# Kernel optimization log

Measured on AMD Instinct MI355X. Metric: run time of the kernel, lower is better.

Reference implementation:

```python
import jax, jax.numpy as jnp
import numpy as np

EPS = 1e-5
SCALE = 0.25
H = 16  # num_heads

def _bn(x, gamma, beta):
    # training-mode BatchNorm1d over (batch, length) per channel; x: [M, C, N]
    mean = jnp.mean(x, axis=(0, 2), keepdims=True)
    var = jnp.var(x, axis=(0, 2), keepdims=True)
    return gamma[None, :, None] * (x - mean) * jax.lax.rsqrt(var + EPS) + beta[None, :, None]

def _spike(x, vth):
    # fresh MyNode within one forward: mem = 0/tau + x, spike if >= vth
    return (x >= vth).astype(x.dtype)

def setup_inputs() -> dict:
    key = jax.random.key(0)
    ks = jax.random.split(key, 8)
    T, B, C, N = 4, 1, 256, 1024
    x = jax.random.normal(ks[0], (T, B, C, N), dtype=jnp.float32)
    y = jax.random.normal(ks[1], (T, B, C, N), dtype=jnp.float32)
    def w(k):
        return jax.random.normal(k, (C, C), dtype=jnp.float32) * (1.0 / np.sqrt(C))
    return {
        "x": x, "y": y,
        "Wq": w(ks[2]), "gq": jnp.ones((C,), jnp.float32), "bq": jnp.zeros((C,), jnp.float32),
        "Wk": w(ks[3]), "gk": jnp.ones((C,), jnp.float32), "bk": jnp.zeros((C,), jnp.float32),
        "Wv": w(ks[4]), "gv": jnp.ones((C,), jnp.float32), "bv": jnp.zeros((C,), jnp.float32),
        "Wp": w(ks[5]), "gp": jnp.ones((C,), jnp.float32), "bp": jnp.zeros((C,), jnp.float32),
    }

def reference(x, y, Wq, gq, bq, Wk, gk, bk, Wv, gv, bv, Wp, gp, bp):
    T, B, C, N = x.shape
    D = C // H
    xf = x.reshape(T * B, C, N)
    yf = y.reshape(T * B, C, N)

    def branch(inp, W, g, b, vth):
        h = jnp.einsum('oc,mcn->mon', W, inp)      # conv1x1
        h = _bn(h, g, b)
        s = _spike(h, vth)                          # LIF spike (fresh state)
        # [T,B,C,N] -> split channels into heads -> [T,B,H,N,D]
        return s.reshape(T, B, H, D, N).transpose(0, 1, 2, 4, 3)

    q = branch(xf, Wq, gq, bq, 1.0)
    k = branch(yf, Wk, gk, bk, 1.0)
    v = branch(yf, Wv, gv, bv, 1.0)

    attn = jnp.einsum('tbhnd,tbhmd->tbhnm', q, k)   # [T,B,H,N,N]
    out = jnp.einsum('tbhnm,tbhmd->tbhnd', attn, v) * SCALE

    # [T,B,H,N,D] -> [T,B,C,N]
    out = out.transpose(0, 1, 2, 4, 3).reshape(T, B, C, N)
    out = _spike(out.reshape(T * B, C, N), 0.5)      # attn_lif, v_threshold=0.5
    out = jnp.einsum('oc,mcn->mon', Wp, out)         # proj conv1x1
    out = _spike(_bn(out, gp, bp), 1.0)              # proj_bn + proj_lif
    return out.reshape(T, B, C, N)
```

## Files before the change

### kernel.cpp

```cpp
#include <hip/hip_runtime.h>
#include <cstdint>
#include <cstddef>
#include <cmath>

static constexpr int C = 256;
static constexpr int N = 1024;
static constexpr int M = 4;
static constexpr size_t PLANE = (size_t)M * C * N;

typedef unsigned short u16;
typedef u16      u16x8 __attribute__((ext_vector_type(8)));
typedef u16      u16x4 __attribute__((ext_vector_type(4)));
typedef _Float16 f16x8 __attribute__((ext_vector_type(8)));
typedef float    f32x4 __attribute__((ext_vector_type(4)));

static constexpr int FSTR = 40;
static constexpr size_t LVX = (size_t)8 * 1024 * 256;
static constexpr size_t LVW = (size_t)4 * 256 * 256;


__device__ __forceinline__ void split3(float v, u16 &h0, u16 &h1, u16 &h2)
{
    union { _Float16 f; u16 u; } cv;
    float a0 = (fabsf(v) >= 6.103515625e-05f) ? v : 0.0f;
    cv.f = (_Float16)a0;                 h0 = cv.u;
    float f0 = (float)cv.f;
    float r1 = v - f0;
    cv.f = (_Float16)(r1 * 4096.0f);     h1 = cv.u;
    float f1 = (float)cv.f * 2.44140625e-4f;
    float r2 = r1 - f1;
    cv.f = (_Float16)(r2 * 16777216.0f); h2 = cv.u;
}

__global__ __launch_bounds__(256) void split_pre(
    const float* __restrict__ x, const float* __restrict__ y,
    const float* __restrict__ Wq, const float* __restrict__ Wk,
    const float* __restrict__ Wv, const float* __restrict__ Wp,
    u16* __restrict__ xyT, u16* __restrict__ wsp)
{
    const int z = blockIdx.z, tid = threadIdx.x;
    if (z < 8){
        const float* __restrict__ src = (z < 4) ? (x + (size_t)z * C * N)
                                                : (y + (size_t)(z - 4) * C * N);
        const int n0 = blockIdx.x * 64, c0 = blockIdx.y * 64;
        __shared__ float Ls[64][65];
        const int cr = tid >> 2, q = tid & 3;
        #pragma unroll
        for (int j = 0; j < 4; ++j){
            float4 vv = *(const float4*)(src + (size_t)(c0 + cr) * N + n0 + q * 16 + j * 4);
            *(float4*)&Ls[cr][q * 16 + j * 4] = vv;
        }
        __syncthreads();
        const int nr = tid >> 2, cq = tid & 3;
        u16 h0[16], h1[16], h2[16];
        #pragma unroll
        for (int e = 0; e < 16; ++e)
            split3(Ls[cq * 16 + e][nr], h0[e], h1[e], h2[e]);
        const size_t base = (size_t)z * (1024 * 256) + (size_t)(n0 + nr) * C + c0 + cq * 16;
        u16x8 t0, t1;
        #pragma unroll
        for (int i = 0; i < 8; ++i){ t0[i] = h0[i]; t1[i] = h0[8 + i]; }
        *(u16x8*)(xyT + base) = t0;            *(u16x8*)(xyT + base + 8) = t1;
        #pragma unroll
        for (int i = 0; i < 8; ++i){ t0[i] = h1[i]; t1[i] = h1[8 + i]; }
        *(u16x8*)(xyT + LVX + base) = t0;      *(u16x8*)(xyT + LVX + base + 8) = t1;
        #pragma unroll
        for (int i = 0; i < 8; ++i){ t0[i] = h2[i]; t1[i] = h2[8 + i]; }
        *(u16x8*)(xyT + 2 * LVX + base) = t0;  *(u16x8*)(xyT + 2 * LVX + base + 8) = t1;
    } else {
        const float* __restrict__ Wm = (z == 8) ? Wq : (z == 9) ? Wk : (z == 10) ? Wv : Wp;
        const int idx = ((blockIdx.y * 16 + blockIdx.x) * 256 + tid) * 4;
        float4 vv = *(const float4*)(Wm + idx);
        const size_t base = (size_t)(z - 8) * 65536 + idx;
        u16x4 o0_, o1_, o2_;
        u16 a, b, c2;
        split3(vv.x, a, b, c2); o0_[0]=a; o1_[0]=b; o2_[0]=c2;
        split3(vv.y, a, b, c2); o0_[1]=a; o1_[1]=b; o2_[1]=c2;
        split3(vv.z, a, b, c2); o0_[2]=a; o1_[2]=b; o2_[2]=c2;
        split3(vv.w, a, b, c2); o0_[3]=a; o1_[3]=b; o2_[3]=c2;
        *(u16x4*)(wsp + base) = o0_;
        *(u16x4*)(wsp + LVW + base) = o1_;
        *(u16x4*)(wsp + 2 * LVW + base) = o2_;
    }
}

__global__ __launch_bounds__(256, 1) void gemm_qkv_f16(
    const u16* __restrict__ xyT, const u16* __restrict__ wsp,
    float* __restrict__ hbase)
{
    const int bz = blockIdx.z, br = bz >> 2, m = bz & 3;
    const int plane = (br == 0) ? m : 4 + m;
    const u16* __restrict__ Xl = xyT + (size_t)plane * 1024 * 256;
    const u16* __restrict__ Wl = wsp + (size_t)br * 65536;
    float* __restrict__ H = hbase + (size_t)br * PLANE + (size_t)m * C * N;

    const int n0 = blockIdx.x * 64, o0 = blockIdx.y * 64;
    const int tid = threadIdx.x, lane = tid & 63, w = tid >> 6;
    const int ow = (w & 1) * 32, nw = (w >> 1) * 32, lm = lane & 15, lk = lane >> 4;

    __shared__ __align__(16) u16 As[2][3][64 * FSTR];
    __shared__ __align__(16) u16 Bs[2][3][64 * FSTR];

    f32x4 ah[2][2], am2[2][2], al[2][2];
    double hs[2][2][4];
    #pragma unroll
    for (int i = 0; i < 2; ++i)
        #pragma unroll
        for (int j = 0; j < 2; ++j){
            ah[i][j] = (f32x4){0.f,0.f,0.f,0.f};
            am2[i][j] = (f32x4){0.f,0.f,0.f,0.f};
            al[i][j] = (f32x4){0.f,0.f,0.f,0.f};
            #pragma unroll
            for (int r = 0; r < 4; ++r) hs[i][j][r] = 0.0;
        }

    const int rA = tid >> 2, c8 = (tid & 3) * 8;
    u16x8 aR[3], bR[3];
    #pragma unroll
    for (int lv = 0; lv < 3; ++lv){
        aR[lv] = *(const u16x8*)(Wl + (size_t)lv * LVW + (size_t)(o0 + rA) * C + c8);
        bR[lv] = *(const u16x8*)(Xl + (size_t)lv * LVX + (size_t)(n0 + rA) * C + c8);
    }

    int buf = 0;
    for (int ch = 0; ch < 8; ++ch){
        #pragma unroll
        for (int lv = 0; lv < 3; ++lv){
            *(u16x8*)&As[buf][lv][rA * FSTR + c8] = aR[lv];
            *(u16x8*)&Bs[buf][lv][rA * FSTR + c8] = bR[lv];
        }
        __syncthreads();
        if (ch < 7){
            const int cc = (ch + 1) * 32;
            #pragma unroll
            for (int lv = 0; lv < 3; ++lv){
                aR[lv] = *(const u16x8*)(Wl + (size_t)lv * LVW + (size_t)(o0 + rA) * C + cc + c8);
                bR[lv] = *(const u16x8*)(Xl + (size_t)lv * LVX + (size_t)(n0 + rA) * C + cc + c8);
            }
        }
        f16x8 af[2][3], bf[2][3];
        #pragma unroll
        for (int ot = 0; ot < 2; ++ot)
            #pragma unroll
            for (int lv = 0; lv < 3; ++lv)
                af[ot][lv] = *(const f16x8*)&As[buf][lv][(ow + ot * 16 + lm) * FSTR + lk * 8];
        #pragma unroll
        for (int nt = 0; nt < 2; ++nt)
            #pragma unroll
            for (int lv = 0; lv < 3; ++lv)
                bf[nt][lv] = *(const f16x8*)&Bs[buf][lv][(nw + nt * 16 + lm) * FSTR + lk * 8];
        #pragma unroll
        for (int ot = 0; ot < 2; ++ot)
            #pragma unroll
            for (int nt = 0; nt < 2; ++nt){
                ah[ot][nt]  = __builtin_amdgcn_mfma_f32_16x16x32_f16(af[ot][0], bf[nt][0], ah[ot][nt], 0, 0, 0);
                am2[ot][nt] = __builtin_amdgcn_mfma_f32_16x16x32_f16(af[ot][0], bf[nt][1], am2[ot][nt], 0, 0, 0);
                am2[ot][nt] = __builtin_amdgcn_mfma_f32_16x16x32_f16(af[ot][1], bf[nt][0], am2[ot][nt], 0, 0, 0);
                al[ot][nt]  = __builtin_amdgcn_mfma_f32_16x16x32_f16(af[ot][1], bf[nt][1], al[ot][nt], 0, 0, 0);
                al[ot][nt]  = __builtin_amdgcn_mfma_f32_16x16x32_f16(af[ot][0], bf[nt][2], al[ot][nt], 0, 0, 0);
                al[ot][nt]  = __builtin_amdgcn_mfma_f32_16x16x32_f16(af[ot][2], bf[nt][0], al[ot][nt], 0, 0, 0);
            }
        if (ch & 1){
            #pragma unroll
            for (int ot = 0; ot < 2; ++ot)
                #pragma unroll
                for (int nt = 0; nt < 2; ++nt){
                    #pragma unroll
                    for (int r = 0; r < 4; ++r) hs[ot][nt][r] += (double)ah[ot][nt][r];
                    ah[ot][nt] = (f32x4){0.f,0.f,0.f,0.f};
                }
        }
        buf ^= 1;
    }

    const double S12 = 1.0 / 4096.0, S24 = 1.0 / 16777216.0;
    #pragma unroll
    for (int ot = 0; ot < 2; ++ot)
        #pragma unroll
        for (int nt = 0; nt < 2; ++nt)
            #pragma unroll
            for (int r = 0; r < 4; ++r){
                double hv = hs[ot][nt][r] + (double)am2[ot][nt][r] * S12 + (double)al[ot][nt][r] * S24;
                H[(size_t)(o0 + ow + ot * 16 + (lk * 4 + r)) * N + (n0 + nw + nt * 16 + lm)] = (float)hv;
            }
}

__global__ __launch_bounds__(256) void bnspike_qkv(
    const float* __restrict__ hbase,
    const float* __restrict__ gq, const float* __restrict__ bq,
    const float* __restrict__ gk, const float* __restrict__ bk,
    const float* __restrict__ gv, const float* __restrict__ bv,
    unsigned char* __restrict__ sbase)
{
    const int o = blockIdx.x, br = blockIdx.y;
    const float* __restrict__ h = hbase + (size_t)br * PLANE + (size_t)o * N;
    const int tid = threadIdx.x;

    float4 v[4];
    double s = 0.0, ss = 0.0;
    #pragma unroll
    for (int j = 0; j < 4; ++j){
        v[j] = *(const float4*)(h + (size_t)j * C * N + tid * 4);
        double a = v[j].x, b = v[j].y, c = v[j].z, d = v[j].w;
        s  += (a + b) + (c + d);
        ss += (a * a + b * b) + (c * c + d * d);
    }
    #pragma unroll
    for (int off = 32; off > 0; off >>= 1){
        s  += __shfl_down(s, off, 64);
        ss += __shfl_down(ss, off, 64);
    }
    __shared__ double rs[4], rss[4], sstat[2];
    const int lane = tid & 63, wv_ = tid >> 6;
    if (lane == 0){ rs[wv_] = s; rss[wv_] = ss; }
    __syncthreads();
    if (tid == 0){
        double S  = rs[0] + rs[1] + rs[2] + rs[3];
        double SS = rss[0] + rss[1] + rss[2] + rss[3];
        double mean = S / 4096.0;
        double var  = SS / 4096.0 - mean * mean;
        sstat[0] = mean;
        sstat[1] = 1.0 / sqrt(var + 1e-5);
    }
    __syncthreads();
    const double mean = sstat[0], inv = sstat[1];
    const float* g = (br == 0) ? gq : (br == 1) ? gk : gv;
    const float* b = (br == 0) ? bq : (br == 1) ? bk : bv;
    const double gc = (double)g[o], bc = (double)b[o];
    unsigned char* out = sbase + (size_t)br * PLANE + (size_t)o * N;
    #pragma unroll
    for (int j = 0; j < 4; ++j){
        unsigned int pk = 0;
        pk |= ((gc * ((double)v[j].x - mean) * inv + bc >= 1.0) ? 1u : 0u);
        pk |= ((gc * ((double)v[j].y - mean) * inv + bc >= 1.0) ? 1u : 0u) << 8;
        pk |= ((gc * ((double)v[j].z - mean) * inv + bc >= 1.0) ? 1u : 0u) << 16;
        pk |= ((gc * ((double)v[j].w - mean) * inv + bc >= 1.0) ? 1u : 0u) << 24;
        *(unsigned int*)(out + (size_t)j * C * N + tid * 4) = pk;
    }
}

__global__ __launch_bounds__(256) void attn_kernel(
    const unsigned char* __restrict__ qb, const unsigned char* __restrict__ kb,
    const unsigned char* __restrict__ vb, unsigned char* __restrict__ s2T)
{
    const int nc = blockIdx.x;
    const int hh = blockIdx.y;
    const int t  = blockIdx.z;
    const int tid = threadIdx.x;

    __shared__ unsigned int kw[16][257];
    __shared__ unsigned int vw[16][257];
    __shared__ int kt[256];

    #pragma unroll
    for (int j = 0; j < 4; ++j){
        int idx = j * 256 + tid;
        int r = idx >> 6, q4 = idx & 63;
        size_t goff = ((size_t)(t * C + hh * 16 + r)) * N + (size_t)q4 * 16;
        uint4 kk = *(const uint4*)(kb + goff);
        uint4 vv = *(const uint4*)(vb + goff);
        kw[r][q4 * 4 + 0] = kk.x; kw[r][q4 * 4 + 1] = kk.y;
        kw[r][q4 * 4 + 2] = kk.z; kw[r][q4 * 4 + 3] = kk.w;
        vw[r][q4 * 4 + 0] = vv.x; vw[r][q4 * 4 + 1] = vv.y;
        vw[r][q4 * 4 + 2] = vv.z; vw[r][q4 * 4 + 3] = vv.w;
    }
    __syncthreads();

    const int d = tid >> 4, dp = tid & 15;
    int sum = 0;
    #pragma unroll 8
    for (int wd = 0; wd < 256; ++wd)
        sum += __popc(kw[d][wd] & vw[dp][wd]);
    kt[tid] = sum;
    __syncthreads();

    const int n = nc * 256 + tid;
    int sums[16];
    #pragma unroll
    for (int i = 0; i < 16; ++i) sums[i] = 0;
    #pragma unroll
    for (int d2 = 0; d2 < 16; ++d2){
        int qv = (int)qb[((size_t)(t * C + hh * 16 + d2)) * N + n];
        #pragma unroll
        for (int dp2 = 0; dp2 < 16; ++dp2)
            sums[dp2] += qv * kt[d2 * 16 + dp2];
    }
    uint4 ov;
    unsigned int* ovp = (unsigned int*)&ov;
    #pragma unroll
    for (int g = 0; g < 4; ++g){
        unsigned int wv2 = 0;
        #pragma unroll
        for (int e = 0; e < 4; ++e)
            wv2 |= ((sums[g * 4 + e] >= 2) ? 1u : 0u) << (8 * e);
        ovp[g] = wv2;
    }
    *(uint4*)(s2T + ((size_t)t * N + n) * C + hh * 16) = ov;
}

__global__ __launch_bounds__(256, 2) void gemm_p_f16(
    const u16* __restrict__ wsp, const unsigned char* __restrict__ s2T,
    float* __restrict__ hp)
{
    const int m = blockIdx.z;
    const int n0 = blockIdx.x * 64, o0 = blockIdx.y * 32;
    const int tid = threadIdx.x, lane = tid & 63, w = tid >> 6;
    const int ow = (w & 1) * 16, nw = (w >> 1) * 32, lm = lane & 15, lk = lane >> 4;
    const u16* __restrict__ Wl = wsp + (size_t)3 * 65536;
    const unsigned char* __restrict__ Xb = s2T + (size_t)m * N * C;
    float* __restrict__ H = hp + (size_t)m * C * N;

    __shared__ __align__(16) u16 As[2][3][32 * FSTR];
    __shared__ __align__(16) u16 Bs[2][64 * FSTR];

    f32x4 a0[2], a1[2], a2[2];
    double hs[2][4];
    #pragma unroll
    for (int i = 0; i < 2; ++i){
        a0[i] = (f32x4){0.f,0.f,0.f,0.f};
        a1[i] = (f32x4){0.f,0.f,0.f,0.f};
        a2[i] = (f32x4){0.f,0.f,0.f,0.f};
        #pragma unroll
        for (int r = 0; r < 4; ++r) hs[i][r] = 0.0;
    }

    const int rA = tid >> 3, c4 = (tid & 7) * 4;
    const int rB = tid >> 2, c8 = (tid & 3) * 8;
    u16x4 aR[3];
    uint2 bw;
    #pragma unroll
    for (int lv = 0; lv < 3; ++lv)
        aR[lv] = *(const u16x4*)(Wl + (size_t)lv * LVW + (size_t)(o0 + rA) * C + c4);
    bw = *(const uint2*)(Xb + (size_t)(n0 + rB) * C + c8);

    int buf = 0;
    for (int ch = 0; ch < 8; ++ch){
        #pragma unroll
        for (int lv = 0; lv < 3; ++lv)
            *(u16x4*)&As[buf][lv][rA * FSTR + c4] = aR[lv];
        u16x8 bv;
        #pragma unroll
        for (int e = 0; e < 4; ++e){
            bv[e]     = (u16)(((bw.x >> (8 * e)) & 1u) * 0x3C00u);
            bv[4 + e] = (u16)(((bw.y >> (8 * e)) & 1u) * 0x3C00u);
        }
        *(u16x8*)&Bs[buf][rB * FSTR + c8] = bv;
        __syncthreads();
        if (ch < 7){
            const int cc = (ch + 1) * 32;
            #pragma unroll
            for (int lv = 0; lv < 3; ++lv)
                aR[lv] = *(const u16x4*)(Wl + (size_t)lv * LVW + (size_t)(o0 + rA) * C + cc + c4);
            bw = *(const uint2*)(Xb + (size_t)(n0 + rB) * C + cc + c8);
        }
        f16x8 af[3], bf[2];
        #pragma unroll
        for (int lv = 0; lv < 3; ++lv)
            af[lv] = *(const f16x8*)&As[buf][lv][(ow + lm) * FSTR + lk * 8];
        #pragma unroll
        for (int nt = 0; nt < 2; ++nt)
            bf[nt] = *(const f16x8*)&Bs[buf][(nw + nt * 16 + lm) * FSTR + lk * 8];
        #pragma unroll
        for (int nt = 0; nt < 2; ++nt){
            a0[nt] = __builtin_amdgcn_mfma_f32_16x16x32_f16(af[0], bf[nt], a0[nt], 0, 0, 0);
            a1[nt] = __builtin_amdgcn_mfma_f32_16x16x32_f16(af[1], bf[nt], a1[nt], 0, 0, 0);
            a2[nt] = __builtin_amdgcn_mfma_f32_16x16x32_f16(af[2], bf[nt], a2[nt], 0, 0, 0);
        }
        if (ch & 1){
            #pragma unroll
            for (int nt = 0; nt < 2; ++nt){
                #pragma unroll
                for (int r = 0; r < 4; ++r) hs[nt][r] += (double)a0[nt][r];
                a0[nt] = (f32x4){0.f,0.f,0.f,0.f};
            }
        }
        buf ^= 1;
    }

    const double S12 = 1.0 / 4096.0, S24 = 1.0 / 16777216.0;
    #pragma unroll
    for (int nt = 0; nt < 2; ++nt)
        #pragma unroll
        for (int r = 0; r < 4; ++r){
            double hv = hs[nt][r] + (double)a1[nt][r] * S12 + (double)a2[nt][r] * S24;
            H[(size_t)(o0 + ow + (lk * 4 + r)) * N + (n0 + nw + nt * 16 + lm)] = (float)hv;
        }
}

__global__ __launch_bounds__(256) void bnspike_p(
    const float* __restrict__ hp,
    const float* __restrict__ gp, const float* __restrict__ bp,
    float* __restrict__ outp)
{
    const int o = blockIdx.x;
    const float* __restrict__ h = hp + (size_t)o * N;
    const int tid = threadIdx.x;

    float4 v[4];
    double s = 0.0, ss = 0.0;
    #pragma unroll
    for (int j = 0; j < 4; ++j){
        v[j] = *(const float4*)(h + (size_t)j * C * N + tid * 4);
        double a = v[j].x, b = v[j].y, c = v[j].z, d = v[j].w;
        s  += (a + b) + (c + d);
        ss += (a * a + b * b) + (c * c + d * d);
    }
    #pragma unroll
    for (int off = 32; off > 0; off >>= 1){
        s  += __shfl_down(s, off, 64);
        ss += __shfl_down(ss, off, 64);
    }
    __shared__ double rs[4], rss[4], sstat[2];
    const int lane = tid & 63, wv_ = tid >> 6;
    if (lane == 0){ rs[wv_] = s; rss[wv_] = ss; }
    __syncthreads();
    if (tid == 0){
        double S  = rs[0] + rs[1] + rs[2] + rs[3];
        double SS = rss[0] + rss[1] + rss[2] + rss[3];
        double mean = S / 4096.0;
        double var  = SS / 4096.0 - mean * mean;
        sstat[0] = mean;
        sstat[1] = 1.0 / sqrt(var + 1e-5);
    }
    __syncthreads();
    const double mean = sstat[0], inv = sstat[1];
    const double gc = (double)gp[o], bc = (double)bp[o];
    float* out = outp + (size_t)o * N;
    #pragma unroll
    for (int j = 0; j < 4; ++j){
        float4 r;
        r.x = (gc * ((double)v[j].x - mean) * inv + bc >= 1.0) ? 1.0f : 0.0f;
        r.y = (gc * ((double)v[j].y - mean) * inv + bc >= 1.0) ? 1.0f : 0.0f;
        r.z = (gc * ((double)v[j].z - mean) * inv + bc >= 1.0) ? 1.0f : 0.0f;
        r.w = (gc * ((double)v[j].w - mean) * inv + bc >= 1.0) ? 1.0f : 0.0f;
        *(float4*)(out + (size_t)j * C * N + tid * 4) = r;
    }
}

extern "C" void kernel_launch(void* const* d_in, const int* in_sizes, int n_in,
                              void* d_out, int out_size, void* d_ws, size_t ws_size,
                              hipStream_t stream)
{
    const float* x  = (const float*)d_in[0];
    const float* y  = (const float*)d_in[1];
    const float* Wq = (const float*)d_in[2];
    const float* gq = (const float*)d_in[3];
    const float* bq = (const float*)d_in[4];
    const float* Wk = (const float*)d_in[5];
    const float* gk = (const float*)d_in[6];
    const float* bk = (const float*)d_in[7];
    const float* Wv = (const float*)d_in[8];
    const float* gv = (const float*)d_in[9];
    const float* bv = (const float*)d_in[10];
    const float* Wp = (const float*)d_in[11];
    const float* gp = (const float*)d_in[12];
    const float* bp = (const float*)d_in[13];
    float* out = (float*)d_out;

    char* ws = (char*)d_ws;
    u16* xyT = (u16*)ws;
    u16* wsp = (u16*)(ws + (size_t)12 * 1024 * 1024);
    float* hq = (float*)(ws + (size_t)14 * 1024 * 1024);
    float* hp = hq;
    unsigned char* qb  = (unsigned char*)ws;
    unsigned char* kb2 = qb + PLANE;
    unsigned char* vb2 = qb + 2 * PLANE;
    unsigned char* s2b = qb + 3 * PLANE;

    split_pre<<<dim3(16, 4, 12), 256, 0, stream>>>(x, y, Wq, Wk, Wv, Wp, xyT, wsp);
    gemm_qkv_f16<<<dim3(16, 4, 12), 256, 0, stream>>>(xyT, wsp, hq);
    bnspike_qkv<<<dim3(256, 3), 256, 0, stream>>>(hq, gq, bq, gk, bk, gv, bv, qb);
    attn_kernel<<<dim3(4, 16, 4), 256, 0, stream>>>(qb, kb2, vb2, s2b);
    gemm_p_f16<<<dim3(16, 8, 4), 256, 0, stream>>>(wsp, s2b, hp);
    bnspike_p<<<dim3(256), 256, 0, stream>>>(hp, gp, bp, out);
}
```

Before: 129.2 us.

## Fuse projection BN-spike into GEMM via grid barrier; load weights directly in QKV GEMM

```diff
diff --git a/kernel.cpp b/kernel.cpp
--- a/kernel.cpp
+++ b/kernel.cpp
@@ -98,7 +98,6 @@
     const int tid = threadIdx.x, lane = tid & 63, w = tid >> 6;
     const int ow = (w & 1) * 32, nw = (w >> 1) * 32, lm = lane & 15, lk = lane >> 4;
 
-    __shared__ __align__(16) u16 As[2][3][64 * FSTR];
     __shared__ __align__(16) u16 Bs[2][3][64 * FSTR];
 
     f32x4 ah[2][2], am2[2][2], al[2][2];
@@ -114,36 +113,34 @@
             for (int r = 0; r < 4; ++r) hs[i][j][r] = 0.0;
         }
 
-    const int rA = tid >> 2, c8 = (tid & 3) * 8;
-    u16x8 aR[3], bR[3];
-    #pragma unroll
-    for (int lv = 0; lv < 3; ++lv){
-        aR[lv] = *(const u16x8*)(Wl + (size_t)lv * LVW + (size_t)(o0 + rA) * C + c8);
-        bR[lv] = *(const u16x8*)(Xl + (size_t)lv * LVX + (size_t)(n0 + rA) * C + c8);
-    }
+    const int rS = tid >> 2, c8 = (tid & 3) * 8;
+    const u16* __restrict__ A0 = Wl + (size_t)(o0 + ow + lm) * C + lk * 8;
+
+    u16x8 bR[3];
+    #pragma unroll
+    for (int lv = 0; lv < 3; ++lv)
+        bR[lv] = *(const u16x8*)(Xl + (size_t)lv * LVX + (size_t)(n0 + rS) * C + c8);
 
     int buf = 0;
     for (int ch = 0; ch < 8; ++ch){
         #pragma unroll
-        for (int lv = 0; lv < 3; ++lv){
-            *(u16x8*)&As[buf][lv][rA * FSTR + c8] = aR[lv];
-            *(u16x8*)&Bs[buf][lv][rA * FSTR + c8] = bR[lv];
-        }
+        for (int lv = 0; lv < 3; ++lv)
+            *(u16x8*)&Bs[buf][lv][rS * FSTR + c8] = bR[lv];
         __syncthreads();
+        const int cco = ch * 32;
+        f16x8 af[2][3];
+        #pragma unroll
+        for (int ot = 0; ot < 2; ++ot)
+            #pragma unroll
+            for (int lv = 0; lv < 3; ++lv)
+                af[ot][lv] = *(const f16x8*)(A0 + (size_t)ot * 16 * C + (size_t)lv * LVW + cco);
         if (ch < 7){
             const int cc = (ch + 1) * 32;
             #pragma unroll
-            for (int lv = 0; lv < 3; ++lv){
-                aR[lv] = *(const u16x8*)(Wl + (size_t)lv * LVW + (size_t)(o0 + rA) * C + cc + c8);
-                bR[lv] = *(const u16x8*)(Xl + (size_t)lv * LVX + (size_t)(n0 + rA) * C + cc + c8);
-            }
-        }
-        f16x8 af[2][3], bf[2][3];
-        #pragma unroll
-        for (int ot = 0; ot < 2; ++ot)
-            #pragma unroll
             for (int lv = 0; lv < 3; ++lv)
-                af[ot][lv] = *(const f16x8*)&As[buf][lv][(ow + ot * 16 + lm) * FSTR + lk * 8];
+                bR[lv] = *(const u16x8*)(Xl + (size_t)lv * LVX + (size_t)(n0 + rS) * C + cc + c8);
+        }
+        f16x8 bf[2][3];
         #pragma unroll
         for (int nt = 0; nt < 2; ++nt)
             #pragma unroll
@@ -241,12 +238,19 @@
 
 __global__ __launch_bounds__(256) void attn_kernel(
     const unsigned char* __restrict__ qb, const unsigned char* __restrict__ kb,
-    const unsigned char* __restrict__ vb, unsigned char* __restrict__ s2T)
+    const unsigned char* __restrict__ vb, unsigned char* __restrict__ s2T,
+    double* __restrict__ pst, unsigned int* __restrict__ cnt)
 {
     const int nc = blockIdx.x;
     const int hh = blockIdx.y;
     const int t  = blockIdx.z;
     const int tid = threadIdx.x;
+
+    if (nc == 0 && hh == 0 && t == 0){
+        pst[tid] = 0.0;
+        pst[tid + 256] = 0.0;
+        if (tid == 0) *cnt = 0u;
+    }
 
     __shared__ unsigned int kw[16][257];
     __shared__ unsigned int vw[16][257];
@@ -298,9 +302,11 @@
     *(uint4*)(s2T + ((size_t)t * N + n) * C + hh * 16) = ov;
 }
 
-__global__ __launch_bounds__(256, 2) void gemm_p_f16(
+__global__ __launch_bounds__(256, 2) void gemm_p_fused(
     const u16* __restrict__ wsp, const unsigned char* __restrict__ s2T,
-    float* __restrict__ hp)
+    const float* __restrict__ gp, const float* __restrict__ bp,
+    double* __restrict__ pst, unsigned int* __restrict__ cnt,
+    float* __restrict__ outp)
 {
     const int m = blockIdx.z;
     const int n0 = blockIdx.x * 64, o0 = blockIdx.y * 32;
@@ -308,7 +314,6 @@
     const int ow = (w & 1) * 16, nw = (w >> 1) * 32, lm = lane & 15, lk = lane >> 4;
     const u16* __restrict__ Wl = wsp + (size_t)3 * 65536;
     const unsigned char* __restrict__ Xb = s2T + (size_t)m * N * C;
-    float* __restrict__ H = hp + (size_t)m * C * N;
 
     __shared__ __align__(16) u16 As[2][3][32 * FSTR];
     __shared__ __align__(16) u16 Bs[2][64 * FSTR];
@@ -378,62 +383,49 @@
     }
 
     const double S12 = 1.0 / 4096.0, S24 = 1.0 / 16777216.0;
+    double hv[2][4];
     #pragma unroll
     for (int nt = 0; nt < 2; ++nt)
         #pragma unroll
-        for (int r = 0; r < 4; ++r){
-            double hv = hs[nt][r] + (double)a1[nt][r] * S12 + (double)a2[nt][r] * S24;
-            H[(size_t)(o0 + ow + (lk * 4 + r)) * N + (n0 + nw + nt * 16 + lm)] = (float)hv;
-        }
-}
-
-__global__ __launch_bounds__(256) void bnspike_p(
-    const float* __restrict__ hp,
-    const float* __restrict__ gp, const float* __restrict__ bp,
-    float* __restrict__ outp)
-{
-    const int o = blockIdx.x;
-    const float* __restrict__ h = hp + (size_t)o * N;
-    const int tid = threadIdx.x;
-
-    float4 v[4];
-    double s = 0.0, ss = 0.0;
-    #pragma unroll
-    for (int j = 0; j < 4; ++j){
-        v[j] = *(const float4*)(h + (size_t)j * C * N + tid * 4);
-        double a = v[j].x, b = v[j].y, c = v[j].z, d = v[j].w;
-        s  += (a + b) + (c + d);
-        ss += (a * a + b * b) + (c * c + d * d);
-    }
-    #pragma unroll
-    for (int off = 32; off > 0; off >>= 1){
-        s  += __shfl_down(s, off, 64);
-        ss += __shfl_down(ss, off, 64);
-    }
-    __shared__ double rs[4], rss[4], sstat[2];
-    const int lane = tid & 63, wv_ = tid >> 6;
-    if (lane == 0){ rs[wv_] = s; rss[wv_] = ss; }
+        for (int r = 0; r < 4; ++r)
+            hv[nt][r] = hs[nt][r] + (double)a1[nt][r] * S12 + (double)a2[nt][r] * S24;
+
+    #pragma unroll
+    for (int r = 0; r < 4; ++r){
+        double s  = hv[0][r] + hv[1][r];
+        double ss = hv[0][r] * hv[0][r] + hv[1][r] * hv[1][r];
+        #pragma unroll
+        for (int off = 1; off < 16; off <<= 1){
+            s  += __shfl_xor(s, off, 64);
+            ss += __shfl_xor(ss, off, 64);
+        }
+        if (lm == 0){
+            const int chn = o0 + ow + lk * 4 + r;
+            atomicAdd(&pst[chn * 2 + 0], s);
+            atomicAdd(&pst[chn * 2 + 1], ss);
+        }
+    }
+    __threadfence();
+    if (tid == 0){
+        __hip_atomic_fetch_add(cnt, 1u, __ATOMIC_ACQ_REL, __HIP_MEMORY_SCOPE_AGENT);
+        while (__hip_atomic_load(cnt, __ATOMIC_ACQUIRE, __HIP_MEMORY_SCOPE_AGENT) < 512u)
+            __builtin_amdgcn_s_sleep(8);
+    }
     __syncthreads();
-    if (tid == 0){
-        double S  = rs[0] + rs[1] + rs[2] + rs[3];
-        double SS = rss[0] + rss[1] + rss[2] + rss[3];
+
+    #pragma unroll
+    for (int r = 0; r < 4; ++r){
+        const int chn = o0 + ow + lk * 4 + r;
+        double S  = __hip_atomic_load(&pst[chn * 2 + 0], __ATOMIC_RELAXED, __HIP_MEMORY_SCOPE_AGENT);
+        double SS = __hip_atomic_load(&pst[chn * 2 + 1], __ATOMIC_RELAXED, __HIP_MEMORY_SCOPE_AGENT);
         double mean = S / 4096.0;
-        double var  = SS / 4096.0 - mean * mean;
-        sstat[0] = mean;
-        sstat[1] = 1.0 / sqrt(var + 1e-5);
-    }
-    __syncthreads();
-    const double mean = sstat[0], inv = sstat[1];
-    const double gc = (double)gp[o], bc = (double)bp[o];
-    float* out = outp + (size_t)o * N;
-    #pragma unroll
-    for (int j = 0; j < 4; ++j){
-        float4 r;
-        r.x = (gc * ((double)v[j].x - mean) * inv + bc >= 1.0) ? 1.0f : 0.0f;
-        r.y = (gc * ((double)v[j].y - mean) * inv + bc >= 1.0) ? 1.0f : 0.0f;
-        r.z = (gc * ((double)v[j].z - mean) * inv + bc >= 1.0) ? 1.0f : 0.0f;
-        r.w = (gc * ((double)v[j].w - mean) * inv + bc >= 1.0) ? 1.0f : 0.0f;
-        *(float4*)(out + (size_t)j * C * N + tid * 4) = r;
+        double inv  = 1.0 / sqrt(SS / 4096.0 - mean * mean + 1e-5);
+        double gc = (double)gp[chn], bc = (double)bp[chn];
+        float* orow = outp + (size_t)m * C * N + (size_t)chn * N;
+        #pragma unroll
+        for (int nt = 0; nt < 2; ++nt)
+            orow[n0 + nw + nt * 16 + lm] =
+                (gc * (hv[nt][r] - mean) * inv + bc >= 1.0) ? 1.0f : 0.0f;
     }
 }
 
@@ -460,8 +452,9 @@
     char* ws = (char*)d_ws;
     u16* xyT = (u16*)ws;
     u16* wsp = (u16*)(ws + (size_t)12 * 1024 * 1024);
+    double* pst = (double*)(ws + (size_t)13 * 1024 * 1024 + 512 * 1024);
+    unsigned int* cnt = (unsigned int*)(pst + 512);
     float* hq = (float*)(ws + (size_t)14 * 1024 * 1024);
-    float* hp = hq;
     unsigned char* qb  = (unsigned char*)ws;
     unsigned char* kb2 = qb + PLANE;
     unsigned char* vb2 = qb + 2 * PLANE;
@@ -470,7 +463,6 @@
     split_pre<<<dim3(16, 4, 12), 256, 0, stream>>>(x, y, Wq, Wk, Wv, Wp, xyT, wsp);
     gemm_qkv_f16<<<dim3(16, 4, 12), 256, 0, stream>>>(xyT, wsp, hq);
     bnspike_qkv<<<dim3(256, 3), 256, 0, stream>>>(hq, gq, bq, gk, bk, gv, bv, qb);
-    attn_kernel<<<dim3(4, 16, 4), 256, 0, stream>>>(qb, kb2, vb2, s2b);
-    gemm_p_f16<<<dim3(16, 8, 4), 256, 0, stream>>>(wsp, s2b, hp);
-    bnspike_p<<<dim3(256), 256, 0, stream>>>(hp, gp, bp, out);
-}
+    attn_kernel<<<dim3(4, 16, 4), 256, 0, stream>>>(qb, kb2, vb2, s2b, pst, cnt);
+    gemm_p_fused<<<dim3(16, 8, 4), 256, 0, stream>>>(wsp, s2b, gp, bp, pst, cnt, out);
+}
```

After: 191.5 us. 1.48x slower.
